# Kernel tuning notes

Hardware: AMD Instinct MI355X
Metric: run time of the kernel (lower is better)

Reference implementation:

```python
import jax, jax.numpy as jnp
import numpy as np

# hyperparameters (from init_kwargs)
A_LOG = 1.0
B_LOG = 1.0
C_LOG = 1.0
THR = 0.5
DT = 1.0
EPS = 1e-5


@jax.custom_vjp
def spike(v_scaled):
    # Heaviside forward, fast-sigmoid surrogate backward
    return (v_scaled > 0).astype(jnp.float32)

def _spike_fwd(v_scaled):
    return spike(v_scaled), v_scaled

def _spike_bwd(v_scaled, dy):
    return (dy / (1.0 + 100.0 * jnp.abs(v_scaled)) ** 2,)

spike.defvjp(_spike_fwd, _spike_bwd)


def setup_inputs() -> dict:
    key = jax.random.key(0)
    k1, k2, k3 = jax.random.split(key, 3)
    T, B, N_IN, N_REC = 1000, 128, 256, 256
    x = jax.random.normal(k1, (T, B, N_IN), dtype=jnp.float32)
    z0 = jnp.zeros((B, N_REC), dtype=jnp.float32)
    v0 = jnp.zeros((B, N_REC), dtype=jnp.float32)
    t0 = jnp.zeros((B, N_REC), dtype=jnp.float32)
    # RandomNormal(stddev=0.01) init for input weights
    w_in = 0.01 * jax.random.normal(k2, (N_IN, N_REC), dtype=jnp.float32)
    # recurrence enabled: small random recurrent weights
    w_rec = 0.01 * jax.random.normal(k3, (N_REC, N_REC), dtype=jnp.float32)
    return {"x": x, "z0": z0, "v0": v0, "t0": t0, "w_in": w_in, "w_rec": w_rec}


def _step(carry, x_t, w_in, w_rec):
    z, v, t = carry                              # each [B, n_rec]
    i_in = x_t @ w_in + z @ w_rec                # [B, n_rec]
    h = (i_in != 0).astype(jnp.float32)          # activity flag
    new_t = t + (1.0 - h)                        # (h != 1) == 1 - h since h in {0,1}
    new_v = v * (1.0 - z)                        # reset on spike
    low_pass = (new_v > -1.0).astype(jnp.float32)
    new_v = new_v - (1.0 - low_pass) * (new_v + 1.0)   # clamp at -1
    # logarithmic leak
    cap = (jnp.exp2(jnp.abs(new_v) / C_LOG) - B_LOG) / A_LOG
    arg = jnp.minimum(DT * h * (new_t + 1.0), cap)
    new_v = new_v - jnp.sign(new_v) * C_LOG * jnp.log2(EPS + A_LOG * arg + B_LOG)
    new_v = new_v + i_in
    new_t = new_t * (1.0 - h)
    new_z = spike((new_v - THR) / THR)
    return (new_z, new_v, new_t), (new_z, new_v)


def reference(x, z0, v0, t0, w_in, w_rec):
    def step(carry, x_t):
        return _step(carry, x_t, w_in, w_rec)
    _, (zs, vs) = jax.lax.scan(step, (z0, v0, t0), x)
    return zs, vs  # each [T, B, n_rec]
```

## Files before the change

### kernel.cpp

```cpp
#include <hip/hip_runtime.h>

__global__ __launch_bounds__(256) void gemm_xw(const float* __restrict__ X,
                                               const float* __restrict__ W,
                                               float* __restrict__ Y,
                                               int M) {
    __shared__ float As[32][132];
    __shared__ float Bs[32][128];

    const int tid = threadIdx.x;
    const int mb = blockIdx.x >> 1;
    const int nb = blockIdx.x & 1;
    const int m0 = mb << 7;
    const int n0 = nb << 7;
    const int tr = (tid >> 4) << 3;
    const int tc = (tid & 15) << 3;

    float acc[8][8];
#pragma unroll
    for (int i = 0; i < 8; ++i)
#pragma unroll
        for (int j = 0; j < 8; ++j) acc[i][j] = 0.f;

    for (int kb = 0; kb < 256; kb += 32) {
#pragma unroll
        for (int i = 0; i < 4; ++i) {
            int f = tid + (i << 8);
            int row = f >> 3, kq = f & 7;
            float4 a = *(const float4*)(X + (size_t)(m0 + row) * 256 + kb + (kq << 2));
            As[(kq << 2) + 0][row] = a.x;
            As[(kq << 2) + 1][row] = a.y;
            As[(kq << 2) + 2][row] = a.z;
            As[(kq << 2) + 3][row] = a.w;
            int rowb = f >> 5, cq = f & 31;
            *(float4*)&Bs[rowb][cq << 2] =
                *(const float4*)(W + (size_t)(kb + rowb) * 256 + n0 + (cq << 2));
        }
        __syncthreads();
#pragma unroll
        for (int k = 0; k < 32; ++k) {
            float a[8], b[8];
            *(float4*)&a[0] = *(const float4*)&As[k][tr];
            *(float4*)&a[4] = *(const float4*)&As[k][tr + 4];
            *(float4*)&b[0] = *(const float4*)&Bs[k][tc];
            *(float4*)&b[4] = *(const float4*)&Bs[k][tc + 4];
#pragma unroll
            for (int i = 0; i < 8; ++i)
#pragma unroll
                for (int j = 0; j < 8; ++j)
                    acc[i][j] = fmaf(a[i], b[j], acc[i][j]);
        }
        __syncthreads();
    }
#pragma unroll
    for (int i = 0; i < 8; ++i) {
        float* yp = Y + (size_t)(m0 + tr + i) * 256 + n0 + tc;
        *(float4*)yp = make_float4(acc[i][0], acc[i][1], acc[i][2], acc[i][3]);
        *(float4*)(yp + 4) = make_float4(acc[i][4], acc[i][5], acc[i][6], acc[i][7]);
    }
}

__global__ __launch_bounds__(64) void lif_seq(const float* __restrict__ ix,
                                              const float* __restrict__ wrec,
                                              const float* __restrict__ z0,
                                              const float* __restrict__ v0,
                                              const float* __restrict__ t0,
                                              float* __restrict__ zs,
                                              float* __restrict__ vs,
                                              int T, int B) {
    const int b = blockIdx.x;
    const int lane = threadIdx.x;
    const int nbase = lane << 2;
    const size_t sb = (size_t)b * 256 + nbase;
    const size_t stride = (size_t)B * 256;

    float4 v4 = *(const float4*)(v0 + sb);
    float4 t4 = *(const float4*)(t0 + sb);
    float4 z4 = *(const float4*)(z0 + sb);
    float v[4] = {v4.x, v4.y, v4.z, v4.w};
    float t[4] = {t4.x, t4.y, t4.z, t4.w};
    bool sp[4] = {z4.x != 0.f, z4.y != 0.f, z4.z != 0.f, z4.w != 0.f};

    const float* ixp = ix + sb;

    auto wload = [&](int row) -> float4 {
        const float* wp = wrec + ((size_t)row << 8) + nbase;
        float4 w4;
        asm volatile("global_load_dwordx4 %0, %1, off\n\ts_waitcnt vmcnt(0)"
                     : "=v"(w4) : "v"(wp) : "memory");
        return w4;
    };

    constexpr float G0 = 1e-5f + 1.0f;

    auto step = [&](float4 r, float4& zo4, float4& vo4) {
        unsigned long long mk0 = __ballot(sp[0]);
        unsigned long long mk1 = __ballot(sp[1]);
        unsigned long long mk2 = __ballot(sp[2]);
        unsigned long long mk3 = __ballot(sp[3]);

        float ir[4] = {0.f, 0.f, 0.f, 0.f};
        if (mk0 | mk1 | mk2 | mk3) {
            unsigned long long mm;
            mm = mk0;
            while (mm) { int j = __builtin_ctzll(mm); mm &= mm - 1;
                float4 w = wload((j << 2) + 0);
                ir[0] += w.x; ir[1] += w.y; ir[2] += w.z; ir[3] += w.w; }
            mm = mk1;
            while (mm) { int j = __builtin_ctzll(mm); mm &= mm - 1;
                float4 w = wload((j << 2) + 1);
                ir[0] += w.x; ir[1] += w.y; ir[2] += w.z; ir[3] += w.w; }
            mm = mk2;
            while (mm) { int j = __builtin_ctzll(mm); mm &= mm - 1;
                float4 w = wload((j << 2) + 2);
                ir[0] += w.x; ir[1] += w.y; ir[2] += w.z; ir[3] += w.w; }
            mm = mk3;
            while (mm) { int j = __builtin_ctzll(mm); mm &= mm - 1;
                float4 w = wload((j << 2) + 3);
                ir[0] += w.x; ir[1] += w.y; ir[2] += w.z; ir[3] += w.w; }
        }

        float rr[4] = {r.x, r.y, r.z, r.w};
        float i_in[4], tp1[4], cT[4], ntn[4], vc[4], E[4], cA[4], L[4], nv[4];
        bool hz[4], spn[4];
        float zf[4];

#pragma unroll
        for (int c = 0; c < 4; ++c) i_in[c] = rr[c] + ir[c];
#pragma unroll
        for (int c = 0; c < 4; ++c) hz[c] = (i_in[c] == 0.f);
#pragma unroll
        for (int c = 0; c < 4; ++c) tp1[c] = t[c] + 1.f;
#pragma unroll
        for (int c = 0; c < 4; ++c) cT[c] = hz[c] ? G0 : ((1e-5f + tp1[c]) + 1.f);
#pragma unroll
        for (int c = 0; c < 4; ++c) ntn[c] = hz[c] ? tp1[c] : 0.f;
#pragma unroll
        for (int c = 0; c < 4; ++c) vc[c] = fmaxf(sp[c] ? 0.f : v[c], -1.f);
#pragma unroll
        for (int c = 0; c < 4; ++c) E[c] = __builtin_amdgcn_exp2f(fabsf(vc[c]));
#pragma unroll
        for (int c = 0; c < 4; ++c) cA[c] = (1e-5f + (E[c] - 1.f)) + 1.f;
#pragma unroll
        for (int c = 0; c < 4; ++c) L[c] = __builtin_amdgcn_logf(fminf(cT[c], cA[c]));
#pragma unroll
        for (int c = 0; c < 4; ++c) {
            float Ls = copysignf(L[c], vc[c]);
            float nvp = (vc[c] == 0.f) ? vc[c] : (vc[c] - Ls);
            nv[c] = nvp + i_in[c];
        }
#pragma unroll
        for (int c = 0; c < 4; ++c) spn[c] = (nv[c] > 0.5f);
#pragma unroll
        for (int c = 0; c < 4; ++c) zf[c] = spn[c] ? 1.f : 0.f;
#pragma unroll
        for (int c = 0; c < 4; ++c) { v[c] = nv[c]; t[c] = ntn[c]; sp[c] = spn[c]; }

        zo4 = make_float4(zf[0], zf[1], zf[2], zf[3]);
        vo4 = make_float4(nv[0], nv[1], nv[2], nv[3]);
    };

    float4 iA[8], iB[8];
    float4 zo[8], vo[8];

    auto loadChunk = [&](float4 (&ib)[8], int c0) {
#pragma unroll
        for (int u = 0; u < 8; ++u) {
            int r = c0 + u;
            r = (r < T) ? r : T - 1;
            ib[u] = *(const float4*)(ixp + (size_t)r * stride);
        }
    };

    auto runChunk = [&](float4 (&ib)[8], int c0) {
#pragma unroll
        for (int u = 0; u < 8; ++u) step(ib[u], zo[u], vo[u]);
        size_t ob = (size_t)c0 * stride + sb;
#pragma unroll
        for (int u = 0; u < 8; ++u) {
            *(float4*)(zs + ob + (size_t)u * stride) = zo[u];
            *(float4*)(vs + ob + (size_t)u * stride) = vo[u];
        }
    };

    loadChunk(iA, 0);
    int c = 0;
    while (c + 16 <= T) {
        loadChunk(iB, c + 8);
        runChunk(iA, c);
        loadChunk(iA, c + 16);
        runChunk(iB, c + 8);
        c += 16;
    }
    if (c + 8 <= T) {
        runChunk(iA, c);
        c += 8;
    }
    for (int ts = c; ts < T; ++ts) {
        float4 r = *(const float4*)(ixp + (size_t)ts * stride);
        float4 zz, vv;
        step(r, zz, vv);
        size_t o = (size_t)ts * stride + sb;
        *(float4*)(zs + o) = zz;
        *(float4*)(vs + o) = vv;
    }
}

extern "C" void kernel_launch(void* const* d_in, const int* in_sizes, int n_in,
                              void* d_out, int out_size, void* d_ws, size_t ws_size,
                              hipStream_t stream) {
    const float* x    = (const float*)d_in[0];
    const float* z0   = (const float*)d_in[1];
    const float* v0   = (const float*)d_in[2];
    const float* t0   = (const float*)d_in[3];
    const float* w_in = (const float*)d_in[4];
    const float* wrec = (const float*)d_in[5];

    const int n_rec = 256;
    const int B = in_sizes[1] / n_rec;
    const int nin = in_sizes[4] / n_rec;
    const int T = in_sizes[0] / (B * nin);
    const int M = T * B;

    float* zs = (float*)d_out;
    float* vs = zs + (size_t)T * B * n_rec;
    float* ixbuf = zs;

    gemm_xw<<<dim3((M / 128) * 2), dim3(256), 0, stream>>>(x, w_in, ixbuf, M);
    lif_seq<<<dim3(B), dim3(64), 0, stream>>>(ixbuf, wrec, z0, v0, t0, zs, vs, T, B);
}
```

Before: 496.7 us.

## Process two batch rows per wavefront in the sequential LIF kernel

Each 64-lane block now handles two batch rows, so the grid halves to B/2 blocks and each lane carries 8 neuron states instead of 4. The two rows' elementwise leak math is interleaved, giving more independent instructions per step to hide the latency of the serial recurrence. The input prefetch chunk shrinks from 8 to 4 steps to limit register use. In exchange, fewer blocks run (64 on a large GPU), each lane does twice the work, and the spike-driven weight gathers for both rows run one after another.

```diff
diff --git a/kernel.cpp b/kernel.cpp
--- a/kernel.cpp
+++ b/kernel.cpp
@@ -67,20 +67,24 @@
                                               float* __restrict__ zs,
                                               float* __restrict__ vs,
                                               int T, int B) {
-    const int b = blockIdx.x;
+    const int b0 = blockIdx.x << 1;
     const int lane = threadIdx.x;
     const int nbase = lane << 2;
-    const size_t sb = (size_t)b * 256 + nbase;
+    const size_t sbA = (size_t)b0 * 256 + nbase;
+    const size_t sbB = (size_t)(b0 + 1) * 256 + nbase;
     const size_t stride = (size_t)B * 256;
 
-    float4 v4 = *(const float4*)(v0 + sb);
-    float4 t4 = *(const float4*)(t0 + sb);
-    float4 z4 = *(const float4*)(z0 + sb);
-    float v[4] = {v4.x, v4.y, v4.z, v4.w};
-    float t[4] = {t4.x, t4.y, t4.z, t4.w};
-    bool sp[4] = {z4.x != 0.f, z4.y != 0.f, z4.z != 0.f, z4.w != 0.f};
-
-    const float* ixp = ix + sb;
+    float v[8], t[8];
+    bool sp[8];
+    {
+        float4 a;
+        a = *(const float4*)(v0 + sbA); v[0]=a.x; v[1]=a.y; v[2]=a.z; v[3]=a.w;
+        a = *(const float4*)(v0 + sbB); v[4]=a.x; v[5]=a.y; v[6]=a.z; v[7]=a.w;
+        a = *(const float4*)(t0 + sbA); t[0]=a.x; t[1]=a.y; t[2]=a.z; t[3]=a.w;
+        a = *(const float4*)(t0 + sbB); t[4]=a.x; t[5]=a.y; t[6]=a.z; t[7]=a.w;
+        a = *(const float4*)(z0 + sbA); sp[0]=a.x!=0.f; sp[1]=a.y!=0.f; sp[2]=a.z!=0.f; sp[3]=a.w!=0.f;
+        a = *(const float4*)(z0 + sbB); sp[4]=a.x!=0.f; sp[5]=a.y!=0.f; sp[6]=a.z!=0.f; sp[7]=a.w!=0.f;
+    }
 
     auto wload = [&](int row) -> float4 {
         const float* wp = wrec + ((size_t)row << 8) + nbase;
@@ -92,116 +96,144 @@
 
     constexpr float G0 = 1e-5f + 1.0f;
 
-    auto step = [&](float4 r, float4& zo4, float4& vo4) {
-        unsigned long long mk0 = __ballot(sp[0]);
-        unsigned long long mk1 = __ballot(sp[1]);
-        unsigned long long mk2 = __ballot(sp[2]);
-        unsigned long long mk3 = __ballot(sp[3]);
-
-        float ir[4] = {0.f, 0.f, 0.f, 0.f};
-        if (mk0 | mk1 | mk2 | mk3) {
+    auto step2 = [&](float4 rA, float4 rB,
+                     float4& zoA, float4& voA, float4& zoB, float4& voB) {
+        unsigned long long mk[8];
+#pragma unroll
+        for (int e = 0; e < 8; ++e) mk[e] = __ballot(sp[e]);
+
+        float rr[8] = {rA.x, rA.y, rA.z, rA.w, rB.x, rB.y, rB.z, rB.w};
+
+        if (mk[0] | mk[1] | mk[2] | mk[3]) {
+            float i0 = 0.f, i1 = 0.f, i2 = 0.f, i3 = 0.f;
             unsigned long long mm;
-            mm = mk0;
+            mm = mk[0];
             while (mm) { int j = __builtin_ctzll(mm); mm &= mm - 1;
                 float4 w = wload((j << 2) + 0);
-                ir[0] += w.x; ir[1] += w.y; ir[2] += w.z; ir[3] += w.w; }
-            mm = mk1;
+                i0 += w.x; i1 += w.y; i2 += w.z; i3 += w.w; }
+            mm = mk[1];
             while (mm) { int j = __builtin_ctzll(mm); mm &= mm - 1;
                 float4 w = wload((j << 2) + 1);
-                ir[0] += w.x; ir[1] += w.y; ir[2] += w.z; ir[3] += w.w; }
-            mm = mk2;
+                i0 += w.x; i1 += w.y; i2 += w.z; i3 += w.w; }
+            mm = mk[2];
             while (mm) { int j = __builtin_ctzll(mm); mm &= mm - 1;
                 float4 w = wload((j << 2) + 2);
-                ir[0] += w.x; ir[1] += w.y; ir[2] += w.z; ir[3] += w.w; }
-            mm = mk3;
+                i0 += w.x; i1 += w.y; i2 += w.z; i3 += w.w; }
+            mm = mk[3];
             while (mm) { int j = __builtin_ctzll(mm); mm &= mm - 1;
                 float4 w = wload((j << 2) + 3);
-                ir[0] += w.x; ir[1] += w.y; ir[2] += w.z; ir[3] += w.w; }
-        }
-
-        float rr[4] = {r.x, r.y, r.z, r.w};
-        float i_in[4], tp1[4], cT[4], ntn[4], vc[4], E[4], cA[4], L[4], nv[4];
-        bool hz[4], spn[4];
-        float zf[4];
-
-#pragma unroll
-        for (int c = 0; c < 4; ++c) i_in[c] = rr[c] + ir[c];
-#pragma unroll
-        for (int c = 0; c < 4; ++c) hz[c] = (i_in[c] == 0.f);
-#pragma unroll
-        for (int c = 0; c < 4; ++c) tp1[c] = t[c] + 1.f;
-#pragma unroll
-        for (int c = 0; c < 4; ++c) cT[c] = hz[c] ? G0 : ((1e-5f + tp1[c]) + 1.f);
-#pragma unroll
-        for (int c = 0; c < 4; ++c) ntn[c] = hz[c] ? tp1[c] : 0.f;
-#pragma unroll
-        for (int c = 0; c < 4; ++c) vc[c] = fmaxf(sp[c] ? 0.f : v[c], -1.f);
-#pragma unroll
-        for (int c = 0; c < 4; ++c) E[c] = __builtin_amdgcn_exp2f(fabsf(vc[c]));
-#pragma unroll
-        for (int c = 0; c < 4; ++c) cA[c] = (1e-5f + (E[c] - 1.f)) + 1.f;
-#pragma unroll
-        for (int c = 0; c < 4; ++c) L[c] = __builtin_amdgcn_logf(fminf(cT[c], cA[c]));
-#pragma unroll
-        for (int c = 0; c < 4; ++c) {
-            float Ls = copysignf(L[c], vc[c]);
-            float nvp = (vc[c] == 0.f) ? vc[c] : (vc[c] - Ls);
-            nv[c] = nvp + i_in[c];
-        }
-#pragma unroll
-        for (int c = 0; c < 4; ++c) spn[c] = (nv[c] > 0.5f);
-#pragma unroll
-        for (int c = 0; c < 4; ++c) zf[c] = spn[c] ? 1.f : 0.f;
-#pragma unroll
-        for (int c = 0; c < 4; ++c) { v[c] = nv[c]; t[c] = ntn[c]; sp[c] = spn[c]; }
-
-        zo4 = make_float4(zf[0], zf[1], zf[2], zf[3]);
-        vo4 = make_float4(nv[0], nv[1], nv[2], nv[3]);
-    };
-
-    float4 iA[8], iB[8];
-    float4 zo[8], vo[8];
-
-    auto loadChunk = [&](float4 (&ib)[8], int c0) {
-#pragma unroll
-        for (int u = 0; u < 8; ++u) {
+                i0 += w.x; i1 += w.y; i2 += w.z; i3 += w.w; }
+            rr[0] += i0; rr[1] += i1; rr[2] += i2; rr[3] += i3;
+        }
+        if (mk[4] | mk[5] | mk[6] | mk[7]) {
+            float i0 = 0.f, i1 = 0.f, i2 = 0.f, i3 = 0.f;
+            unsigned long long mm;
+            mm = mk[4];
+            while (mm) { int j = __builtin_ctzll(mm); mm &= mm - 1;
+                float4 w = wload((j << 2) + 0);
+                i0 += w.x; i1 += w.y; i2 += w.z; i3 += w.w; }
+            mm = mk[5];
+            while (mm) { int j = __builtin_ctzll(mm); mm &= mm - 1;
+                float4 w = wload((j << 2) + 1);
+                i0 += w.x; i1 += w.y; i2 += w.z; i3 += w.w; }
+            mm = mk[6];
+            while (mm) { int j = __builtin_ctzll(mm); mm &= mm - 1;
+                float4 w = wload((j << 2) + 2);
+                i0 += w.x; i1 += w.y; i2 += w.z; i3 += w.w; }
+            mm = mk[7];
+            while (mm) { int j = __builtin_ctzll(mm); mm &= mm - 1;
+                float4 w = wload((j << 2) + 3);
+                i0 += w.x; i1 += w.y; i2 += w.z; i3 += w.w; }
+            rr[4] += i0; rr[5] += i1; rr[6] += i2; rr[7] += i3;
+        }
+
+        float tp1[8], cT[8], ntn[8], vc[8], E[8], cA[8], L[8], nv[8], zf[8];
+        bool hz[8], spn[8];
+#pragma unroll
+        for (int e = 0; e < 8; ++e) hz[e] = (rr[e] == 0.f);
+#pragma unroll
+        for (int e = 0; e < 8; ++e) tp1[e] = t[e] + 1.f;
+#pragma unroll
+        for (int e = 0; e < 8; ++e) cT[e] = hz[e] ? G0 : ((1e-5f + tp1[e]) + 1.f);
+#pragma unroll
+        for (int e = 0; e < 8; ++e) ntn[e] = hz[e] ? tp1[e] : 0.f;
+#pragma unroll
+        for (int e = 0; e < 8; ++e) vc[e] = fmaxf(sp[e] ? 0.f : v[e], -1.f);
+#pragma unroll
+        for (int e = 0; e < 8; ++e) E[e] = __builtin_amdgcn_exp2f(fabsf(vc[e]));
+#pragma unroll
+        for (int e = 0; e < 8; ++e) cA[e] = (1e-5f + (E[e] - 1.f)) + 1.f;
+#pragma unroll
+        for (int e = 0; e < 8; ++e) L[e] = __builtin_amdgcn_logf(fminf(cT[e], cA[e]));
+#pragma unroll
+        for (int e = 0; e < 8; ++e) {
+            float Ls = copysignf(L[e], vc[e]);
+            float nvp = (vc[e] == 0.f) ? vc[e] : (vc[e] - Ls);
+            nv[e] = nvp + rr[e];
+        }
+#pragma unroll
+        for (int e = 0; e < 8; ++e) spn[e] = (nv[e] > 0.5f);
+#pragma unroll
+        for (int e = 0; e < 8; ++e) zf[e] = spn[e] ? 1.f : 0.f;
+#pragma unroll
+        for (int e = 0; e < 8; ++e) { v[e] = nv[e]; t[e] = ntn[e]; sp[e] = spn[e]; }
+
+        zoA = make_float4(zf[0], zf[1], zf[2], zf[3]);
+        voA = make_float4(nv[0], nv[1], nv[2], nv[3]);
+        zoB = make_float4(zf[4], zf[5], zf[6], zf[7]);
+        voB = make_float4(nv[4], nv[5], nv[6], nv[7]);
+    };
+
+    float4 iA0[4], iB0[4], iA1[4], iB1[4];
+    float4 zoA[4], voA[4], zoB[4], voB[4];
+
+    auto loadChunk = [&](float4 (&bA)[4], float4 (&bB)[4], int c0) {
+#pragma unroll
+        for (int u = 0; u < 4; ++u) {
             int r = c0 + u;
             r = (r < T) ? r : T - 1;
-            ib[u] = *(const float4*)(ixp + (size_t)r * stride);
-        }
-    };
-
-    auto runChunk = [&](float4 (&ib)[8], int c0) {
-#pragma unroll
-        for (int u = 0; u < 8; ++u) step(ib[u], zo[u], vo[u]);
-        size_t ob = (size_t)c0 * stride + sb;
-#pragma unroll
-        for (int u = 0; u < 8; ++u) {
-            *(float4*)(zs + ob + (size_t)u * stride) = zo[u];
-            *(float4*)(vs + ob + (size_t)u * stride) = vo[u];
-        }
-    };
-
-    loadChunk(iA, 0);
+            bA[u] = *(const float4*)(ix + (size_t)r * stride + sbA);
+            bB[u] = *(const float4*)(ix + (size_t)r * stride + sbB);
+        }
+    };
+
+    auto runChunk = [&](float4 (&bA)[4], float4 (&bB)[4], int c0) {
+#pragma unroll
+        for (int u = 0; u < 4; ++u)
+            step2(bA[u], bB[u], zoA[u], voA[u], zoB[u], voB[u]);
+#pragma unroll
+        for (int u = 0; u < 4; ++u) {
+            size_t o = (size_t)(c0 + u) * stride;
+            *(float4*)(zs + o + sbA) = zoA[u];
+            *(float4*)(vs + o + sbA) = voA[u];
+            *(float4*)(zs + o + sbB) = zoB[u];
+            *(float4*)(vs + o + sbB) = voB[u];
+        }
+    };
+
+    loadChunk(iA0, iB0, 0);
     int c = 0;
-    while (c + 16 <= T) {
-        loadChunk(iB, c + 8);
-        runChunk(iA, c);
-        loadChunk(iA, c + 16);
-        runChunk(iB, c + 8);
-        c += 16;
-    }
-    if (c + 8 <= T) {
-        runChunk(iA, c);
+    while (c + 8 <= T) {
+        loadChunk(iA1, iB1, c + 4);
+        runChunk(iA0, iB0, c);
+        loadChunk(iA0, iB0, c + 8);
+        runChunk(iA1, iB1, c + 4);
         c += 8;
     }
+    if (c + 4 <= T) {
+        runChunk(iA0, iB0, c);
+        c += 4;
+    }
     for (int ts = c; ts < T; ++ts) {
-        float4 r = *(const float4*)(ixp + (size_t)ts * stride);
-        float4 zz, vv;
-        step(r, zz, vv);
-        size_t o = (size_t)ts * stride + sb;
-        *(float4*)(zs + o) = zz;
-        *(float4*)(vs + o) = vv;
+        float4 rA = *(const float4*)(ix + (size_t)ts * stride + sbA);
+        float4 rB = *(const float4*)(ix + (size_t)ts * stride + sbB);
+        float4 za, va, zb, vb;
+        step2(rA, rB, za, va, zb, vb);
+        size_t o = (size_t)ts * stride;
+        *(float4*)(zs + o + sbA) = za;
+        *(float4*)(vs + o + sbA) = va;
+        *(float4*)(zs + o + sbB) = zb;
+        *(float4*)(vs + o + sbB) = vb;
     }
 }
 
@@ -226,5 +258,5 @@
     float* ixbuf = zs;
 
     gemm_xw<<<dim3((M / 128) * 2), dim3(256), 0, stream>>>(x, w_in, ixbuf, M);
-    lif_seq<<<dim3(B), dim3(64), 0, stream>>>(ixbuf, wrec, z0, v0, t0, zs, vs, T, B);
+    lif_seq<<<dim3(B >> 1), dim3(64), 0, stream>>>(ixbuf, wrec, z0, v0, t0, zs, vs, T, B);
 }
```

Result: slower. 779.3 us (+56.9%).
